# Kernel tuning notes

Measured on AMD Instinct MI355X. Metric: run time of the kernel, lower is better.

## Reference

```python
import jax, jax.numpy as jnp
import numpy as np

B, NB, K, L, S, V = 32, 688, 4, 688, 688, 50
PAD = 0
TEMP = 0.1
SMOOTH = 0.1
L_CLS, L_PTR, L_EMPTY, L_ROW, L_COL = 1.0, 1.0, 1.0, 0.5, 0.5


def setup_inputs() -> dict:
    key = jax.random.key(0)
    ks = jax.random.split(key, 12)
    tag_logits = jax.random.normal(ks[0], (B, S, V), jnp.float32)
    tag_targets = jax.random.randint(ks[1], (B, S), 0, V)
    pointer_logits = jax.random.normal(ks[2], (B, NB, S), jnp.float32)
    # targets only on even OTSL positions (which we mark as data tags below)
    raw = jax.random.randint(ks[3], (B, NB, K), 0, S // 2) * 2
    drop = jax.random.uniform(ks[4], (B, NB, K)) < 0.25
    box_indices = jnp.where(drop, -1, raw)
    pos = jnp.arange(S)
    data_otsl = jnp.broadcast_to(pos % 2 == 0, (B, S))
    empty_otsl = (pos % 2 == 1)[None, :] & (jax.random.uniform(ks[5], (B, S)) < 0.5)
    zeros_prompt = jnp.zeros((B, L), bool)
    data_tag_mask = jnp.concatenate([zeros_prompt, data_otsl], axis=1)
    empty_tag_mask = jnp.concatenate([zeros_prompt, empty_otsl], axis=1)
    empty_pointer_logits = jax.random.normal(ks[6], (B, 1, S), jnp.float32)
    row_sim_matrix = jax.random.normal(ks[7], (B, NB, NB), jnp.float32)
    col_sim_matrix = jax.random.normal(ks[8], (B, NB, NB), jnp.float32)

    def make_coef(k):
        k1, k2 = jax.random.split(k)
        c = jax.random.uniform(k1, (B, NB, NB))
        inv = jax.random.uniform(k2, (B, NB, NB)) < 0.1
        return jnp.where(inv, -1.0, c)

    row_span_coef = make_coef(ks[9])
    col_span_coef = make_coef(ks[10])
    return dict(tag_logits=tag_logits, tag_targets=tag_targets,
                pointer_logits=pointer_logits, box_indices=box_indices,
                data_tag_mask=data_tag_mask, empty_tag_mask=empty_tag_mask,
                empty_pointer_logits=empty_pointer_logits,
                row_sim_matrix=row_sim_matrix, col_sim_matrix=col_sim_matrix,
                row_span_coef=row_span_coef, col_span_coef=col_span_coef)


def _tag_loss(tag_logits, tag_targets):
    logp = jax.nn.log_softmax(tag_logits, axis=-1).reshape(-1, V)
    t = tag_targets.reshape(-1)
    valid = t != PAD
    nll = -jnp.take_along_axis(logp, jnp.where(valid, t, 0)[:, None], axis=1)[:, 0]
    smooth = -logp.mean(axis=-1)
    per = (1.0 - SMOOTH) * nll + SMOOTH * smooth
    return (per * valid).sum() / valid.sum()


def _pointer_loss(pointer_logits, box_indices, data_tag_mask):
    log_probs = jax.nn.log_softmax(pointer_logits / TEMP, axis=-1)  # (B,NB,S)
    valid_pos = data_tag_mask[:, L:]  # (B,S)
    log_probs = jnp.where(valid_pos[:, None, :], log_probs, -jnp.inf)
    valid = box_indices != -1  # (B,NB,K)
    safe = jnp.where(valid, box_indices, 0)
    g = jnp.take_along_axis(log_probs, safe, axis=-1)  # (B,NB,K)
    g = jnp.where(valid, g, 0.0)
    cnt = valid.sum(axis=-1)  # (B,NB)
    has = cnt > 0
    per = -(g.sum(axis=-1) / jnp.maximum(cnt, 1))
    total = (per * has).sum()
    return total / (has.sum() + 1e-6)


def _empty_ptr_loss(empty_logits, data_tag_mask, empty_tag_mask):
    x = empty_logits[:, 0, :]  # (B,S)
    otsl_mask = (data_tag_mask | empty_tag_mask)[:, L:]
    targets = empty_tag_mask[:, L:].astype(jnp.float32)
    # stable BCE with logits
    bce = jnp.maximum(x, 0.0) - x * targets + jnp.log1p(jnp.exp(-jnp.abs(x)))
    masked = bce * otsl_mask
    num_c = otsl_mask.sum(axis=1) + 1e-08
    return (masked.sum(axis=1) / num_c).mean()


def _contrastive_loss(sim, coef):
    s = sim / TEMP
    e = jnp.exp(s)
    lp = jnp.log(e / e.sum(axis=-1, keepdims=True) + 1e-08)
    vm = coef >= 0
    w = coef * lp * vm
    box = -(w.sum(axis=-1) / (coef.sum(axis=-1) + 1e-08))
    vb = vm.any(axis=-1)
    return (box * vb).sum() / (vb.sum() + 1e-08)


def reference(tag_logits, tag_targets, pointer_logits, box_indices,
              data_tag_mask, empty_tag_mask, empty_pointer_logits,
              row_sim_matrix, col_sim_matrix, row_span_coef, col_span_coef):
    cls_loss = _tag_loss(tag_logits, tag_targets)
    ptr_loss = _pointer_loss(pointer_logits, box_indices, data_tag_mask)
    empty_loss = _empty_ptr_loss(empty_pointer_logits, data_tag_mask, empty_tag_mask)
    row_loss = _contrastive_loss(row_sim_matrix, row_span_coef)
    col_loss = _contrastive_loss(col_sim_matrix, col_span_coef)
    total = (L_CLS * cls_loss + L_PTR * ptr_loss + L_EMPTY * empty_loss
             + L_ROW * row_loss + L_COL * col_loss)
    return (total, cls_loss, ptr_loss, empty_loss, row_loss, col_loss)
```

## Files before the change

kernel.cpp:

```cpp
#include <hip/hip_runtime.h>
#include <cstddef>

namespace {

constexpr int B  = 32;
constexpr int NB = 688;
constexpr int K  = 4;
constexpr int L  = 688;
constexpr int S  = 688;
constexpr int V  = 50;
constexpr int LS = L + S;
constexpr int ROWS  = B * NB;
constexpr float TINV = 10.0f;
constexpr int Q3 = S / 4 - 128;

constexpr int NBLK = 2048;

constexpr int A_PT = 0, A_PH = 1, A_RS = 2, A_RV = 3, A_CS = 4,
              A_CV = 5, A_TS = 6, A_TC = 7, A_ES = 8;

__device__ __forceinline__ float wred_sum(float v) {
#pragma unroll
  for (int o = 32; o > 0; o >>= 1) v += __shfl_xor(v, o);
  return v;
}

__device__ __forceinline__ float4 q_exp_t(const float4 v) {
  return make_float4(__expf(v.x * TINV), __expf(v.y * TINV),
                     __expf(v.z * TINV), __expf(v.w * TINV));
}
__device__ __forceinline__ float q_sum(const float4 a) {
  return (a.x + a.y) + (a.z + a.w);
}

__device__ __forceinline__ void c_quad(const float4 e, const float4 c,
                                       float A, float lgz,
                                       float& wsum, float& csum, bool& anyv) {
  csum += ((c.x + c.y) + (c.z + c.w));
  if (c.x >= 0.f) { wsum += c.x * (__logf(e.x + A) - lgz); anyv = true; }
  if (c.y >= 0.f) { wsum += c.y * (__logf(e.y + A) - lgz); anyv = true; }
  if (c.z >= 0.f) { wsum += c.z * (__logf(e.z + A) - lgz); anyv = true; }
  if (c.w >= 0.f) { wsum += c.w * (__logf(e.w + A) - lgz); anyv = true; }
}

__device__ __forceinline__ void con_row(int r, int lane,
    const float* __restrict__ sim, const float* __restrict__ coef,
    float& a0, float& a1)
{
  const float4* sp4 = reinterpret_cast<const float4*>(sim  + (size_t)r * S);
  const float4* cp4 = reinterpret_cast<const float4*>(coef + (size_t)r * S);
  const bool t3 = (lane < Q3);
  float4 v0 = sp4[lane];
  float4 v1 = sp4[lane + 64];
  float4 c0 = cp4[lane];
  float4 c1 = cp4[lane + 64];
  float4 v2 = t3 ? sp4[lane + 128] : make_float4(0, 0, 0, 0);
  float4 c2 = t3 ? cp4[lane + 128] : make_float4(0, 0, 0, 0);

  float4 e0 = q_exp_t(v0);
  float4 e1 = q_exp_t(v1);
  float4 e2 = t3 ? q_exp_t(v2) : make_float4(0, 0, 0, 0);

  float z = q_sum(e0) + q_sum(e1) + q_sum(e2);
  z = wred_sum(z);
  float A   = 1e-8f * z;
  float lgz = __logf(z);

  float wsum = 0.f, csum = 0.f;
  bool  anyv = false;
  c_quad(e0, c0, A, lgz, wsum, csum, anyv);
  c_quad(e1, c1, A, lgz, wsum, csum, anyv);
  if (t3) c_quad(e2, c2, A, lgz, wsum, csum, anyv);

  wsum = wred_sum(wsum);
  csum = wred_sum(csum);
  if (__ballot(anyv)) {
    a0 += -(wsum / (csum + 1e-8f));
    a1 += 1.f;
  }
}

__device__ __forceinline__ void ptr_row(int r, int lane,
    const float* __restrict__ plog, const int* __restrict__ box,
    const int* __restrict__ dmask, float& a0, float& a1)
{
  const float*  pl  = plog + (size_t)r * S;
  const float4* pl4 = reinterpret_cast<const float4*>(pl);
  const bool t3 = (lane < Q3);
  float4 v0 = pl4[lane];
  float4 v1 = pl4[lane + 64];
  float4 v2 = t3 ? pl4[lane + 128] : make_float4(0, 0, 0, 0);
  int idx = (lane < K) ? box[(size_t)r * K + lane] : -1;

  float4 e0 = q_exp_t(v0);
  float4 e1 = q_exp_t(v1);
  float4 e2 = t3 ? q_exp_t(v2) : make_float4(0, 0, 0, 0);
  float z = q_sum(e0) + q_sum(e1) + q_sum(e2);
  z = wred_sum(z);
  float lse = __logf(z);

  bool vld = (idx != -1) & (lane < K);
  float g = 0.f;
  if (vld) {
    int bb = r / NB;
    int vp = dmask[(size_t)bb * LS + L + idx];
    float sv = pl[idx] * TINV;
    g = vp ? (sv - lse) : -INFINITY;
  }
  g += __shfl_xor(g, 1);
  g += __shfl_xor(g, 2);
  unsigned long long bal = __ballot(vld);
  int cnt = __popcll(bal);
  if (cnt > 0) {
    a0 += -(g / (float)cnt);
    a1 += 1.f;
  }
}

__device__ __forceinline__ void tag_row(int row, int lane,
    const float* __restrict__ tl_base, const int* __restrict__ tgt,
    float& a0, float& a1)
{
  const float* tl = tl_base + (size_t)row * V;
  const bool a = (lane < V);
  float xv = a ? tl[lane] : 0.f;
  int   t  = tgt[row];
  float ev = a ? __expf(xv) : 0.f;
  float sx = a ? xv : 0.f;
  float z    = wred_sum(ev);
  float sumx = wred_sum(sx);
  float lse = __logf(z);
  float xt  = __shfl(xv, t);
  if (t != 0) {
    a0 += lse - 0.9f * xt - 0.002f * sumx;
    a1 += 1.f;
  }
}

__device__ __forceinline__ void empty_row(int b, int lane,
    const float* __restrict__ elog, const int* __restrict__ dmask,
    const int* __restrict__ emask, float& a0)
{
  const float* el = elog + (size_t)b * S;
  const int* dm = dmask + (size_t)b * LS + L;
  const int* em = emask + (size_t)b * LS + L;
  float bs = 0.f, bc = 0.f;
  for (int j = lane; j < S; j += 64) {
    float xv = el[j];
    int d = dm[j], e = em[j];
    float tt = (float)e;
    float bce = fmaxf(xv, 0.f) - xv * tt + log1pf(__expf(-fabsf(xv)));
    if (d | e) { bs += bce; bc += 1.f; }
  }
  bs = wred_sum(bs);
  bc = wred_sum(bc);
  a0 += bs / (bc + 1e-8f);
}

__global__ __launch_bounds__(256, 8) void fused_loss(
    const float* __restrict__ tag_logits, const int* __restrict__ tag_targets,
    const float* __restrict__ plog, const int* __restrict__ box,
    const int* __restrict__ dmask, const int* __restrict__ emask,
    const float* __restrict__ elog,
    const float* __restrict__ rsim, const float* __restrict__ csim,
    const float* __restrict__ rcoef, const float* __restrict__ ccoef,
    float* __restrict__ ws)
{
  const int tid  = threadIdx.x;
  const int lane = tid & 63;
  const int wave = tid >> 6;
  const int b    = blockIdx.x;

  const int start = (b * 43) >> 2;
  const int end   = ((b + 1) * 43) >> 2;

  float pt = 0.f, ph = 0.f, rs = 0.f, rv = 0.f, cs = 0.f, cv = 0.f,
        ts = 0.f, tc = 0.f, es = 0.f;

  for (int r = start + wave; r < end; r += 4) {
    con_row(r, lane, rsim, rcoef, rs, rv);
    con_row(r, lane, csim, ccoef, cs, cv);
  }
  for (int r = start + wave; r < end; r += 4) {
    ptr_row(r, lane, plog, box, dmask, pt, ph);
    tag_row(r, lane, tag_logits, tag_targets, ts, tc);
  }
  if (b < B && wave == (b & 3)) empty_row(b, lane, elog, dmask, emask, es);

  __shared__ float sacc[4][9];
  if (lane == 0) {
    sacc[wave][0] = pt; sacc[wave][1] = ph; sacc[wave][2] = rs;
    sacc[wave][3] = rv; sacc[wave][4] = cs; sacc[wave][5] = cv;
    sacc[wave][6] = ts; sacc[wave][7] = tc; sacc[wave][8] = es;
  }
  __syncthreads();
  if (tid < 9) {
    float t0 = sacc[0][tid] + sacc[1][tid] + sacc[2][tid] + sacc[3][tid];
    ws[tid * NBLK + b] = t0;
  }
}

__global__ void combine_kernel(const float* __restrict__ ws,
                               float* __restrict__ out)
{
  const int lane = threadIdx.x;
  double acc[9];
#pragma unroll
  for (int a = 0; a < 9; ++a) acc[a] = 0.0;
  for (int i = lane; i < NBLK; i += 64) {
#pragma unroll
    for (int a = 0; a < 9; ++a) acc[a] += (double)ws[a * NBLK + i];
  }
#pragma unroll
  for (int a = 0; a < 9; ++a) {
#pragma unroll
    for (int o = 32; o > 0; o >>= 1) acc[a] += __shfl_xor(acc[a], o);
  }
  if (lane == 0) {
    float cls  = (float)(acc[A_TS] / acc[A_TC]);
    float ptr  = (float)(acc[A_PT] / (acc[A_PH] + 1e-6));
    float emp  = (float)(acc[A_ES] / (double)B);
    float row  = (float)(acc[A_RS] / (acc[A_RV] + 1e-8));
    float col  = (float)(acc[A_CS] / (acc[A_CV] + 1e-8));
    float total = cls + ptr + emp + 0.5f * row + 0.5f * col;
    out[0] = total; out[1] = cls; out[2] = ptr;
    out[3] = emp;   out[4] = row; out[5] = col;
  }
}

}

extern "C" void kernel_launch(void* const* d_in, const int* in_sizes, int n_in,
                              void* d_out, int out_size, void* d_ws, size_t ws_size,
                              hipStream_t stream)
{
  const float* tag_logits  = (const float*)d_in[0];
  const int*   tag_targets = (const int*)  d_in[1];
  const float* plog        = (const float*)d_in[2];
  const int*   box         = (const int*)  d_in[3];
  const int*   dmask       = (const int*)  d_in[4];
  const int*   emask       = (const int*)  d_in[5];
  const float* elog        = (const float*)d_in[6];
  const float* rsim        = (const float*)d_in[7];
  const float* csim        = (const float*)d_in[8];
  const float* rcoef       = (const float*)d_in[9];
  const float* ccoef       = (const float*)d_in[10];

  float* ws  = (float*)d_ws;
  float* out = (float*)d_out;

  fused_loss<<<NBLK, 256, 0, stream>>>(tag_logits, tag_targets, plog, box,
                                       dmask, emask, elog, rsim, csim,
                                       rcoef, ccoef, ws);
  combine_kernel<<<1, 64, 0, stream>>>(ws, out);
}
```

Before: 71.32 us.

## Give each wave a contiguous row range and software-prefetch the next similarity rows

Each wave now takes its own contiguous slice of rows. Before, the four waves of a block interleaved over a shared block range. The contrastive loop now processes the row and column matrices together and prefetches the next row's similarity data while computing the current row. Paired and quad shuffle reductions cut the number of reduction chains. The grid is halved to 1024 blocks with launch bounds relaxed to 4 blocks per SM. Partial sums are written per wave instead of per block, and the combine kernel is widened to 256 threads to handle the four-times-larger partial array. The prefetch raises register pressure, and the smaller grid may leave less latency hiding.

```diff
diff --git a/kernel.cpp b/kernel.cpp
--- a/kernel.cpp
+++ b/kernel.cpp
@@ -10,11 +10,13 @@
 constexpr int S  = 688;
 constexpr int V  = 50;
 constexpr int LS = L + S;
-constexpr int ROWS  = B * NB;
+constexpr int ROWS = B * NB;
 constexpr float TINV = 10.0f;
 constexpr int Q3 = S / 4 - 128;
-
-constexpr int NBLK = 2048;
+constexpr int QR = S / 4;
+
+constexpr int NBLK  = 1024;
+constexpr int NWAVE = NBLK * 4;
 
 constexpr int A_PT = 0, A_PH = 1, A_RS = 2, A_RV = 3, A_CS = 4,
               A_CV = 5, A_TS = 6, A_TC = 7, A_ES = 8;
@@ -23,6 +25,17 @@
 #pragma unroll
   for (int o = 32; o > 0; o >>= 1) v += __shfl_xor(v, o);
   return v;
+}
+__device__ __forceinline__ void wred2(float& a, float& b) {
+#pragma unroll
+  for (int o = 32; o > 0; o >>= 1) { a += __shfl_xor(a, o); b += __shfl_xor(b, o); }
+}
+__device__ __forceinline__ void wred4(float& a, float& b, float& c, float& d) {
+#pragma unroll
+  for (int o = 32; o > 0; o >>= 1) {
+    a += __shfl_xor(a, o); b += __shfl_xor(b, o);
+    c += __shfl_xor(c, o); d += __shfl_xor(d, o);
+  }
 }
 
 __device__ __forceinline__ float4 q_exp_t(const float4 v) {
@@ -31,6 +44,13 @@
 }
 __device__ __forceinline__ float q_sum(const float4 a) {
   return (a.x + a.y) + (a.z + a.w);
+}
+
+__device__ __forceinline__ void load3(const float4* __restrict__ p4, int lane,
+                                      bool t3, float4& a, float4& b, float4& c) {
+  a = p4[lane];
+  b = p4[lane + 64];
+  c = t3 ? p4[lane + 128] : make_float4(0.f, 0.f, 0.f, 0.f);
 }
 
 __device__ __forceinline__ void c_quad(const float4 e, const float4 c,
@@ -43,58 +63,19 @@
   if (c.w >= 0.f) { wsum += c.w * (__logf(e.w + A) - lgz); anyv = true; }
 }
 
-__device__ __forceinline__ void con_row(int r, int lane,
-    const float* __restrict__ sim, const float* __restrict__ coef,
-    float& a0, float& a1)
-{
-  const float4* sp4 = reinterpret_cast<const float4*>(sim  + (size_t)r * S);
-  const float4* cp4 = reinterpret_cast<const float4*>(coef + (size_t)r * S);
-  const bool t3 = (lane < Q3);
-  float4 v0 = sp4[lane];
-  float4 v1 = sp4[lane + 64];
-  float4 c0 = cp4[lane];
-  float4 c1 = cp4[lane + 64];
-  float4 v2 = t3 ? sp4[lane + 128] : make_float4(0, 0, 0, 0);
-  float4 c2 = t3 ? cp4[lane + 128] : make_float4(0, 0, 0, 0);
+__device__ __forceinline__ void ptr_row(int r, int lane, bool t3,
+    const float* __restrict__ plog, const int* __restrict__ box,
+    const int* __restrict__ dmask, float& a0, float& a1)
+{
+  const float*  pl  = plog + (size_t)r * S;
+  const float4* pl4 = reinterpret_cast<const float4*>(pl);
+  float4 v0, v1, v2;
+  load3(pl4, lane, t3, v0, v1, v2);
+  int idx = (lane < K) ? box[(size_t)r * K + lane] : -1;
 
   float4 e0 = q_exp_t(v0);
   float4 e1 = q_exp_t(v1);
-  float4 e2 = t3 ? q_exp_t(v2) : make_float4(0, 0, 0, 0);
-
-  float z = q_sum(e0) + q_sum(e1) + q_sum(e2);
-  z = wred_sum(z);
-  float A   = 1e-8f * z;
-  float lgz = __logf(z);
-
-  float wsum = 0.f, csum = 0.f;
-  bool  anyv = false;
-  c_quad(e0, c0, A, lgz, wsum, csum, anyv);
-  c_quad(e1, c1, A, lgz, wsum, csum, anyv);
-  if (t3) c_quad(e2, c2, A, lgz, wsum, csum, anyv);
-
-  wsum = wred_sum(wsum);
-  csum = wred_sum(csum);
-  if (__ballot(anyv)) {
-    a0 += -(wsum / (csum + 1e-8f));
-    a1 += 1.f;
-  }
-}
-
-__device__ __forceinline__ void ptr_row(int r, int lane,
-    const float* __restrict__ plog, const int* __restrict__ box,
-    const int* __restrict__ dmask, float& a0, float& a1)
-{
-  const float*  pl  = plog + (size_t)r * S;
-  const float4* pl4 = reinterpret_cast<const float4*>(pl);
-  const bool t3 = (lane < Q3);
-  float4 v0 = pl4[lane];
-  float4 v1 = pl4[lane + 64];
-  float4 v2 = t3 ? pl4[lane + 128] : make_float4(0, 0, 0, 0);
-  int idx = (lane < K) ? box[(size_t)r * K + lane] : -1;
-
-  float4 e0 = q_exp_t(v0);
-  float4 e1 = q_exp_t(v1);
-  float4 e2 = t3 ? q_exp_t(v2) : make_float4(0, 0, 0, 0);
+  float4 e2 = t3 ? q_exp_t(v2) : make_float4(0.f, 0.f, 0.f, 0.f);
   float z = q_sum(e0) + q_sum(e1) + q_sum(e2);
   z = wred_sum(z);
   float lse = __logf(z);
@@ -127,12 +108,11 @@
   int   t  = tgt[row];
   float ev = a ? __expf(xv) : 0.f;
   float sx = a ? xv : 0.f;
-  float z    = wred_sum(ev);
-  float sumx = wred_sum(sx);
-  float lse = __logf(z);
+  wred2(ev, sx);
+  float lse = __logf(ev);
   float xt  = __shfl(xv, t);
   if (t != 0) {
-    a0 += lse - 0.9f * xt - 0.002f * sumx;
+    a0 += lse - 0.9f * xt - 0.002f * sx;
     a1 += 1.f;
   }
 }
@@ -152,12 +132,11 @@
     float bce = fmaxf(xv, 0.f) - xv * tt + log1pf(__expf(-fabsf(xv)));
     if (d | e) { bs += bce; bc += 1.f; }
   }
-  bs = wred_sum(bs);
-  bc = wred_sum(bc);
+  wred2(bs, bc);
   a0 += bs / (bc + 1e-8f);
 }
 
-__global__ __launch_bounds__(256, 8) void fused_loss(
+__global__ __launch_bounds__(256, 4) void fused_loss(
     const float* __restrict__ tag_logits, const int* __restrict__ tag_targets,
     const float* __restrict__ plog, const int* __restrict__ box,
     const int* __restrict__ dmask, const int* __restrict__ emask,
@@ -169,59 +148,114 @@
   const int tid  = threadIdx.x;
   const int lane = tid & 63;
   const int wave = tid >> 6;
-  const int b    = blockIdx.x;
-
-  const int start = (b * 43) >> 2;
-  const int end   = ((b + 1) * 43) >> 2;
-
-  float pt = 0.f, ph = 0.f, rs = 0.f, rv = 0.f, cs = 0.f, cv = 0.f,
-        ts = 0.f, tc = 0.f, es = 0.f;
-
-  for (int r = start + wave; r < end; r += 4) {
-    con_row(r, lane, rsim, rcoef, rs, rv);
-    con_row(r, lane, csim, ccoef, cs, cv);
-  }
-  for (int r = start + wave; r < end; r += 4) {
-    ptr_row(r, lane, plog, box, dmask, pt, ph);
-    tag_row(r, lane, tag_logits, tag_targets, ts, tc);
-  }
-  if (b < B && wave == (b & 3)) empty_row(b, lane, elog, dmask, emask, es);
-
-  __shared__ float sacc[4][9];
+  const int wid  = blockIdx.x * 4 + wave;
+  const bool t3  = (lane < Q3);
+
+  const int ws_ = (wid * 43) >> 3;
+  const int we_ = ((wid + 1) * 43) >> 3;
+
+  float aPT = 0.f, aPH = 0.f, aRS = 0.f, aRV = 0.f, aCS = 0.f,
+        aCV = 0.f, aTS = 0.f, aTC = 0.f, aES = 0.f;
+
+  {
+    float4 nr0, nr1, nr2, nm0, nm1, nm2;
+    int r = ws_;
+    if (r < we_) {
+      load3(reinterpret_cast<const float4*>(rsim) + (size_t)r * QR, lane, t3, nr0, nr1, nr2);
+      load3(reinterpret_cast<const float4*>(csim) + (size_t)r * QR, lane, t3, nm0, nm1, nm2);
+    }
+    while (r < we_) {
+      float4 x0 = nr0, x1 = nr1, x2 = nr2;
+      float4 y0 = nm0, y1 = nm1, y2 = nm2;
+      float4 cr0, cr1, cr2, cm0, cm1, cm2;
+      load3(reinterpret_cast<const float4*>(rcoef) + (size_t)r * QR, lane, t3, cr0, cr1, cr2);
+      load3(reinterpret_cast<const float4*>(ccoef) + (size_t)r * QR, lane, t3, cm0, cm1, cm2);
+      const int rn = r + 1;
+      if (rn < we_) {
+        load3(reinterpret_cast<const float4*>(rsim) + (size_t)rn * QR, lane, t3, nr0, nr1, nr2);
+        load3(reinterpret_cast<const float4*>(csim) + (size_t)rn * QR, lane, t3, nm0, nm1, nm2);
+      }
+      x0 = q_exp_t(x0); x1 = q_exp_t(x1);
+      x2 = t3 ? q_exp_t(x2) : make_float4(0.f, 0.f, 0.f, 0.f);
+      y0 = q_exp_t(y0); y1 = q_exp_t(y1);
+      y2 = t3 ? q_exp_t(y2) : make_float4(0.f, 0.f, 0.f, 0.f);
+
+      float zr = q_sum(x0) + q_sum(x1) + q_sum(x2);
+      float zc = q_sum(y0) + q_sum(y1) + q_sum(y2);
+      wred2(zr, zc);
+      const float Ar = 1e-8f * zr, lgzr = __logf(zr);
+      const float Ac = 1e-8f * zc, lgzc = __logf(zc);
+
+      float wr = 0.f, cr = 0.f, wc = 0.f, cc = 0.f;
+      bool anyr = false, anyc = false;
+      c_quad(x0, cr0, Ar, lgzr, wr, cr, anyr);
+      c_quad(y0, cm0, Ac, lgzc, wc, cc, anyc);
+      c_quad(x1, cr1, Ar, lgzr, wr, cr, anyr);
+      c_quad(y1, cm1, Ac, lgzc, wc, cc, anyc);
+      if (t3) {
+        c_quad(x2, cr2, Ar, lgzr, wr, cr, anyr);
+        c_quad(y2, cm2, Ac, lgzc, wc, cc, anyc);
+      }
+      wred4(wr, cr, wc, cc);
+      if (__ballot(anyr)) { aRS += -(wr / (cr + 1e-8f)); aRV += 1.f; }
+      if (__ballot(anyc)) { aCS += -(wc / (cc + 1e-8f)); aCV += 1.f; }
+      r = rn;
+    }
+  }
+
+  for (int r = ws_; r < we_; ++r) {
+    ptr_row(r, lane, t3, plog, box, dmask, aPT, aPH);
+    tag_row(r, lane, tag_logits, tag_targets, aTS, aTC);
+  }
+
+  if (wid < B) empty_row(wid, lane, elog, dmask, emask, aES);
+
   if (lane == 0) {
-    sacc[wave][0] = pt; sacc[wave][1] = ph; sacc[wave][2] = rs;
-    sacc[wave][3] = rv; sacc[wave][4] = cs; sacc[wave][5] = cv;
-    sacc[wave][6] = ts; sacc[wave][7] = tc; sacc[wave][8] = es;
+    ws[A_PT * NWAVE + wid] = aPT;
+    ws[A_PH * NWAVE + wid] = aPH;
+    ws[A_RS * NWAVE + wid] = aRS;
+    ws[A_RV * NWAVE + wid] = aRV;
+    ws[A_CS * NWAVE + wid] = aCS;
+    ws[A_CV * NWAVE + wid] = aCV;
+    ws[A_TS * NWAVE + wid] = aTS;
+    ws[A_TC * NWAVE + wid] = aTC;
+    ws[A_ES * NWAVE + wid] = aES;
+  }
+}
+
+__global__ __launch_bounds__(256) void combine_kernel(
+    const float* __restrict__ ws, float* __restrict__ out)
+{
+  const int tid  = threadIdx.x;
+  const int lane = tid & 63;
+  const int w    = tid >> 6;
+  double acc[9];
+#pragma unroll
+  for (int a = 0; a < 9; ++a) acc[a] = 0.0;
+  for (int i = tid; i < NWAVE; i += 256) {
+#pragma unroll
+    for (int a = 0; a < 9; ++a) acc[a] += (double)ws[a * NWAVE + i];
+  }
+#pragma unroll
+  for (int a = 0; a < 9; ++a) {
+#pragma unroll
+    for (int o = 32; o > 0; o >>= 1) acc[a] += __shfl_xor(acc[a], o);
+  }
+  __shared__ double sh[4][9];
+  if (lane == 0) {
+#pragma unroll
+    for (int a = 0; a < 9; ++a) sh[w][a] = acc[a];
   }
   __syncthreads();
-  if (tid < 9) {
-    float t0 = sacc[0][tid] + sacc[1][tid] + sacc[2][tid] + sacc[3][tid];
-    ws[tid * NBLK + b] = t0;
-  }
-}
-
-__global__ void combine_kernel(const float* __restrict__ ws,
-                               float* __restrict__ out)
-{
-  const int lane = threadIdx.x;
-  double acc[9];
-#pragma unroll
-  for (int a = 0; a < 9; ++a) acc[a] = 0.0;
-  for (int i = lane; i < NBLK; i += 64) {
-#pragma unroll
-    for (int a = 0; a < 9; ++a) acc[a] += (double)ws[a * NBLK + i];
-  }
-#pragma unroll
-  for (int a = 0; a < 9; ++a) {
-#pragma unroll
-    for (int o = 32; o > 0; o >>= 1) acc[a] += __shfl_xor(acc[a], o);
-  }
-  if (lane == 0) {
-    float cls  = (float)(acc[A_TS] / acc[A_TC]);
-    float ptr  = (float)(acc[A_PT] / (acc[A_PH] + 1e-6));
-    float emp  = (float)(acc[A_ES] / (double)B);
-    float row  = (float)(acc[A_RS] / (acc[A_RV] + 1e-8));
-    float col  = (float)(acc[A_CS] / (acc[A_CV] + 1e-8));
+  if (tid == 0) {
+    double t[9];
+#pragma unroll
+    for (int a = 0; a < 9; ++a) t[a] = sh[0][a] + sh[1][a] + sh[2][a] + sh[3][a];
+    float cls  = (float)(t[A_TS] / t[A_TC]);
+    float ptr  = (float)(t[A_PT] / (t[A_PH] + 1e-6));
+    float emp  = (float)(t[A_ES] / (double)B);
+    float row  = (float)(t[A_RS] / (t[A_RV] + 1e-8));
+    float col  = (float)(t[A_CS] / (t[A_CV] + 1e-8));
     float total = cls + ptr + emp + 0.5f * row + 0.5f * col;
     out[0] = total; out[1] = cls; out[2] = ptr;
     out[3] = emp;   out[4] = row; out[5] = col;
@@ -252,5 +286,5 @@
   fused_loss<<<NBLK, 256, 0, stream>>>(tag_logits, tag_targets, plog, box,
                                        dmask, emask, elog, rsim, csim,
                                        rcoef, ccoef, ws);
-  combine_kernel<<<1, 64, 0, stream>>>(ws, out);
-}
+  combine_kernel<<<1, 256, 0, stream>>>(ws, out);
+}
```

Result: no change. 72.37 us (+1.5%).
